# Kernel optimization log

Hardware: AMD Instinct MI355X
Metric: run time of the kernel (lower is better)

## Reference

```python
import jax, jax.numpy as jnp
import numpy as np

N_NODES = 40000
N_EDGES = 640000
IN_C = 128
HID = 32
HEADS = 4
OUT_C = 8
NUM_GRAPHS = 64
NEG_SLOPE = 0.2


def setup_inputs() -> dict:
    key = jax.random.key(0)
    ks = jax.random.split(key, 16)
    x = jax.random.normal(ks[0], (N_NODES, IN_C), dtype=jnp.float32)
    edge_index = jax.random.randint(ks[1], (2, N_EDGES), 0, N_NODES, dtype=jnp.int64)
    batch = jnp.sort(jax.random.randint(ks[2], (N_NODES,), 0, NUM_GRAPHS, dtype=jnp.int64))
    s = lambda k, shape, fan_in: jax.random.normal(k, shape, jnp.float32) / np.sqrt(fan_in)
    # conv0: in -> hid, 4 heads, concat
    W0 = s(ks[3], (IN_C, HEADS * HID), IN_C)
    a_src0 = s(ks[4], (HEADS, HID), HID)
    a_dst0 = s(ks[5], (HEADS, HID), HID)
    b0 = jnp.zeros((HEADS * HID,), jnp.float32)
    # conv1: hid*H -> hid, 4 heads, concat
    W1 = s(ks[6], (HEADS * HID, HEADS * HID), HEADS * HID)
    a_src1 = s(ks[7], (HEADS, HID), HID)
    a_dst1 = s(ks[8], (HEADS, HID), HID)
    b1 = jnp.zeros((HEADS * HID,), jnp.float32)
    # conv2: hid*H -> hid, 1 head, no concat
    W2 = s(ks[9], (HEADS * HID, HID), HEADS * HID)
    a_src2 = s(ks[10], (1, HID), HID)
    a_dst2 = s(ks[11], (1, HID), HID)
    b2 = jnp.zeros((HID,), jnp.float32)
    lin1_w = s(ks[12], (HID, IN_C), HID)
    lin1_b = jnp.zeros((IN_C,), jnp.float32)
    lin2_w = s(ks[13], (IN_C, OUT_C), IN_C)
    lin2_b = jnp.zeros((OUT_C,), jnp.float32)
    return dict(x=x, edge_index=edge_index, batch=batch,
                W0=W0, a_src0=a_src0, a_dst0=a_dst0, b0=b0,
                W1=W1, a_src1=a_src1, a_dst1=a_dst1, b1=b1,
                W2=W2, a_src2=a_src2, a_dst2=a_dst2, b2=b2,
                lin1_w=lin1_w, lin1_b=lin1_b, lin2_w=lin2_w, lin2_b=lin2_b)


def gat_conv(x, src, dst, W, a_src, a_dst, b, heads, out_c, concat):
    N = x.shape[0]
    h = (x @ W).reshape(N, heads, out_c)          # [N,H,C]
    als = (h * a_src[None]).sum(-1)               # [N,H]
    ald = (h * a_dst[None]).sum(-1)               # [N,H]
    e = jax.nn.leaky_relu(als[src] + ald[dst], NEG_SLOPE)  # [E,H]
    m = jax.ops.segment_max(e, dst, num_segments=N)
    m = jnp.where(jnp.isfinite(m), m, 0.0)
    p = jnp.exp(e - m[dst])                       # [E,H]
    denom = jax.ops.segment_sum(p, dst, num_segments=N)
    alpha = p / jnp.maximum(denom[dst], 1e-16)
    out = jax.ops.segment_sum(h[src] * alpha[:, :, None], dst, num_segments=N)
    out = out.reshape(N, heads * out_c) if concat else out.mean(axis=1)
    return out + b


def reference(x, edge_index, batch,
              W0, a_src0, a_dst0, b0,
              W1, a_src1, a_dst1, b1,
              W2, a_src2, a_dst2, b2,
              lin1_w, lin1_b, lin2_w, lin2_b):
    N = x.shape[0]
    # PyG GATConv adds self-loops by default
    loop = jnp.arange(N, dtype=edge_index.dtype)
    src = jnp.concatenate([edge_index[0], loop])
    dst = jnp.concatenate([edge_index[1], loop])
    # eval mode: dropout is identity
    h = jax.nn.elu(gat_conv(x, src, dst, W0, a_src0, a_dst0, b0, HEADS, HID, True))
    h = jax.nn.elu(gat_conv(h, src, dst, W1, a_src1, a_dst1, b1, HEADS, HID, True))
    h = jax.nn.elu(gat_conv(h, src, dst, W2, a_src2, a_dst2, b2, 1, HID, False))
    # global mean pool over graphs
    sums = jax.ops.segment_sum(h, batch, num_segments=NUM_GRAPHS)
    cnts = jax.ops.segment_sum(jnp.ones((N, 1), h.dtype), batch, num_segments=NUM_GRAPHS)
    g = sums / jnp.maximum(cnts, 1.0)             # [G, HID]
    g = jax.nn.relu(g @ lin1_w + lin1_b)
    return g @ lin2_w + lin2_b                    # [G, OUT_C]
```

## Files before the change

kernel.cpp:

```cpp
#include <hip/hip_runtime.h>
#include <hip/hip_bf16.h>

#define N_NODES 40000
#define N_EDGES 640000
#define E_TOT   (N_EDGES + N_NODES)
#define NUM_GRAPHS 64
#define CAP_SHIFT 6

#define CVTX_BLOCKS 5000
#define CVTW_BLOCKS 144
#define CVT_BLOCKS (CVTX_BLOCKS + CVTW_BLOCKS)
#define EBLOCKS ((E_TOT + 255) / 256)
#define GEMM_BLOCKS 625

typedef __attribute__((ext_vector_type(8))) short bf16x8;
typedef __attribute__((ext_vector_type(4))) float f32x4;

__device__ inline float bf2f(unsigned short u) {
    union { unsigned int i; float f; } v; v.i = ((unsigned int)u) << 16; return v.f;
}
__device__ inline unsigned short f2bf(float f) {
    union { float f; unsigned int i; } v; v.f = f;
    unsigned int r = v.i + 0x7FFF + ((v.i >> 16) & 1);
    return (unsigned short)(r >> 16);
}


__global__ __launch_bounds__(256) void cvt_kernel(const float* __restrict__ x,
                                                  const float* __restrict__ W0,
                                                  const float* __restrict__ W1,
                                                  const float* __restrict__ W2,
                                                  unsigned short* __restrict__ Xb,
                                                  unsigned short* __restrict__ Wt0,
                                                  unsigned short* __restrict__ Wt1,
                                                  unsigned short* __restrict__ Wt2) {
    int b = blockIdx.x;
    int tid = threadIdx.x;
    if (b < CVTX_BLOCKS) {
        int i = b * 256 + tid;
        float4 v = ((const float4*)x)[i];
        ushort4 o;
        o.x = f2bf(v.x); o.y = f2bf(v.y); o.z = f2bf(v.z); o.w = f2bf(v.w);
        ((ushort4*)Xb)[i] = o;
    } else {
        int idx = (b - CVTX_BLOCKS) * 256 + tid;
        if (idx < 16384) {
            int n = idx >> 7, k = idx & 127;
            Wt0[idx] = f2bf(W0[k * 128 + n]);
        } else if (idx < 32768) {
            int i = idx - 16384;
            int n = i >> 7, k = i & 127;
            Wt1[i] = f2bf(W1[k * 128 + n]);
        } else if (idx < 36864) {
            int i = idx - 32768;
            int n = i >> 7, k = i & 127;
            Wt2[i] = f2bf(W2[k * 32 + n]);
        }
    }
}


__device__ __forceinline__ void gemm128_body(int blk,
                                             const unsigned short* __restrict__ Xb,
                                             const unsigned short* __restrict__ Wt,
                                             const float* __restrict__ asrc,
                                             const float* __restrict__ adst,
                                             unsigned short* __restrict__ Hb,
                                             float* __restrict__ ALS_t,
                                             float* __restrict__ ALD_t) {
    int wave = threadIdx.x >> 6;
    int lane = threadIdx.x & 63;
    int l15 = lane & 15;
    int q = lane >> 4;
    int r0 = (blk * 4 + wave) * 16;

    f32x4 acc[8];
#pragma unroll
    for (int t = 0; t < 8; ++t) acc[t] = (f32x4){0.f, 0.f, 0.f, 0.f};

    float asv[8], adv[8];
#pragma unroll
    for (int t = 0; t < 8; ++t) {
        int c = t * 16 + l15;
        asv[t] = asrc[c];
        adv[t] = adst[c];
    }

    const unsigned short* xrow = Xb + (long)(r0 + l15) * 128 + q * 8;
    const unsigned short* wrow = Wt + (long)l15 * 128 + q * 8;
#pragma unroll
    for (int kt = 0; kt < 4; ++kt) {
        bf16x8 a = *(const bf16x8*)(xrow + kt * 32);
#pragma unroll
        for (int t = 0; t < 8; ++t) {
            bf16x8 b = *(const bf16x8*)(wrow + (long)t * 16 * 128 + kt * 32);
            acc[t] = __builtin_amdgcn_mfma_f32_16x16x32_bf16(a, b, acc[t], 0, 0, 0);
        }
    }

#pragma unroll
    for (int t = 0; t < 8; ++t)
#pragma unroll
        for (int i = 0; i < 4; ++i)
            Hb[(long)(r0 + q * 4 + i) * 128 + t * 16 + l15] = f2bf(acc[t][i]);

#pragma unroll
    for (int i = 0; i < 4; ++i) {
        float ps0 = acc[0][i] * asv[0] + acc[1][i] * asv[1];
        float ps1 = acc[2][i] * asv[2] + acc[3][i] * asv[3];
        float ps2 = acc[4][i] * asv[4] + acc[5][i] * asv[5];
        float ps3 = acc[6][i] * asv[6] + acc[7][i] * asv[7];
        float pd0 = acc[0][i] * adv[0] + acc[1][i] * adv[1];
        float pd1 = acc[2][i] * adv[2] + acc[3][i] * adv[3];
        float pd2 = acc[4][i] * adv[4] + acc[5][i] * adv[5];
        float pd3 = acc[6][i] * adv[6] + acc[7][i] * adv[7];
#pragma unroll
        for (int m = 1; m < 16; m <<= 1) {
            ps0 += __shfl_xor(ps0, m, 16); ps1 += __shfl_xor(ps1, m, 16);
            ps2 += __shfl_xor(ps2, m, 16); ps3 += __shfl_xor(ps3, m, 16);
            pd0 += __shfl_xor(pd0, m, 16); pd1 += __shfl_xor(pd1, m, 16);
            pd2 += __shfl_xor(pd2, m, 16); pd3 += __shfl_xor(pd3, m, 16);
        }
        int r = r0 + q * 4 + i;
        if (l15 < 4) {
            float v = (l15 == 0) ? ps0 : (l15 == 1) ? ps1 : (l15 == 2) ? ps2 : ps3;
            ALS_t[l15 * N_NODES + r] = v;
        } else if (l15 < 8) {
            int h = l15 - 4;
            float v = (h == 0) ? pd0 : (h == 1) ? pd1 : (h == 2) ? pd2 : pd3;
            ALD_t[h * N_NODES + r] = v;
        }
    }
}


__global__ __launch_bounds__(256) void gemm_scatter_kernel(const unsigned short* __restrict__ Xb,
                                                           const unsigned short* __restrict__ Wt,
                                                           const float* __restrict__ asrc,
                                                           const float* __restrict__ adst,
                                                           unsigned short* __restrict__ Hb,
                                                           float* __restrict__ ALS_t,
                                                           float* __restrict__ ALD_t,
                                                           const int* __restrict__ esrc,
                                                           const int* __restrict__ edst,
                                                           int* __restrict__ cnt,
                                                           int* __restrict__ psrc) {
    int b = blockIdx.x;
    if (b < GEMM_BLOCKS) {
        gemm128_body(b, Xb, Wt, asrc, adst, Hb, ALS_t, ALD_t);
    } else {
        int e = (b - GEMM_BLOCKS) * 256 + threadIdx.x;
        if (e < E_TOT) {
            int d, s;
            if (e < N_EDGES) { d = edst[e]; s = esrc[e]; }
            else             { d = e - N_EDGES; s = d; }
            int slot = atomicAdd(&cnt[d], 1);
            psrc[(d << CAP_SHIFT) + slot] = s;
        }
    }
}

__global__ __launch_bounds__(256) void gemm128_mfma(const unsigned short* __restrict__ Xb,
                                                    const unsigned short* __restrict__ Wt,
                                                    const float* __restrict__ asrc,
                                                    const float* __restrict__ adst,
                                                    unsigned short* __restrict__ Hb,
                                                    float* __restrict__ ALS_t,
                                                    float* __restrict__ ALD_t) {
    gemm128_body(blockIdx.x, Xb, Wt, asrc, adst, Hb, ALS_t, ALD_t);
}

__global__ __launch_bounds__(256) void gemm32_mfma(const unsigned short* __restrict__ Xb,
                                                   const unsigned short* __restrict__ Wt2,
                                                   const float* __restrict__ asrc,
                                                   const float* __restrict__ adst,
                                                   unsigned short* __restrict__ H2b,
                                                   float* __restrict__ ALS,
                                                   float* __restrict__ ALD) {
    int wave = threadIdx.x >> 6;
    int lane = threadIdx.x & 63;
    int l15 = lane & 15;
    int q = lane >> 4;
    int r0 = (blockIdx.x * 4 + wave) * 16;

    f32x4 acc[2];
    acc[0] = (f32x4){0.f, 0.f, 0.f, 0.f};
    acc[1] = (f32x4){0.f, 0.f, 0.f, 0.f};

    const unsigned short* xrow = Xb + (long)(r0 + l15) * 128 + q * 8;
    const unsigned short* wrow = Wt2 + (long)l15 * 128 + q * 8;
#pragma unroll
    for (int kt = 0; kt < 4; ++kt) {
        bf16x8 a = *(const bf16x8*)(xrow + kt * 32);
#pragma unroll
        for (int t = 0; t < 2; ++t) {
            bf16x8 b = *(const bf16x8*)(wrow + (long)t * 16 * 128 + kt * 32);
            acc[t] = __builtin_amdgcn_mfma_f32_16x16x32_bf16(a, b, acc[t], 0, 0, 0);
        }
    }

    float as0 = asrc[l15], as1 = asrc[16 + l15];
    float ad0 = adst[l15], ad1 = adst[16 + l15];
#pragma unroll
    for (int t = 0; t < 2; ++t)
#pragma unroll
        for (int i = 0; i < 4; ++i)
            H2b[(long)(r0 + q * 4 + i) * 32 + t * 16 + l15] = f2bf(acc[t][i]);

#pragma unroll
    for (int i = 0; i < 4; ++i) {
        float ps = acc[0][i] * as0 + acc[1][i] * as1;
        float pd = acc[0][i] * ad0 + acc[1][i] * ad1;
#pragma unroll
        for (int m = 1; m < 16; m <<= 1) {
            ps += __shfl_xor(ps, m, 16);
            pd += __shfl_xor(pd, m, 16);
        }
        if (l15 == 0) {
            int r = r0 + q * 4 + i;
            ALS[r] = ps;
            ALD[r] = pd;
        }
    }
}

__global__ __launch_bounds__(256) void agg128(const unsigned short* __restrict__ Hb,
                                              const float* __restrict__ ALS_t,
                                              const float* __restrict__ ALD_t,
                                              const int* __restrict__ cnt,
                                              const int* __restrict__ psrc,
                                              const float* __restrict__ bias,
                                              unsigned short* __restrict__ OUTb) {
    int n = blockIdx.x * 4 + (threadIdx.x >> 6);
    n = __builtin_amdgcn_readfirstlane(n);
    if (n >= N_NODES) return;
    int lane = threadIdx.x & 63;
    int c = lane * 2;
    int head = lane >> 4;
    int e16 = lane & 15;
    float aldh = ALD_t[head * N_NODES + n];
    const float* alsh = ALS_t + (long)head * N_NODES;
    int j0 = n << CAP_SHIFT;
    int j1 = j0 + __builtin_amdgcn_readfirstlane(cnt[n]);
    float a0 = 0.f, a1 = 0.f, dsum = 0.f;
    for (int jb = j0; jb < j1; jb += 16) {
        int j = jb + e16;
        int jc = (j < j1) ? j : (j1 - 1);
        int s = psrc[jc];
        float e = alsh[s] + aldh;
        e = (e > 0.f) ? e : 0.2f * e;
        float w = (j < j1) ? __expf(e) : 0.f;
        int st[16]; float wt[16];
#pragma unroll
        for (int t = 0; t < 16; ++t) {
            st[t] = __shfl(s, t, 16);
            wt[t] = __shfl(w, t, 16);
        }
        unsigned int hv[16];
#pragma unroll
        for (int t = 0; t < 16; ++t)
            hv[t] = *(const unsigned int*)(Hb + (long)st[t] * 128 + c);
#pragma unroll
        for (int t = 0; t < 16; ++t) {
            float h0 = bf2f((unsigned short)(hv[t] & 0xFFFF));
            float h1 = bf2f((unsigned short)(hv[t] >> 16));
            dsum += wt[t];
            a0 += wt[t] * h0;
            a1 += wt[t] * h1;
        }
    }
    float inv = 1.0f / dsum;
    float o0 = a0 * inv + bias[c];
    float o1 = a1 * inv + bias[c + 1];
    o0 = (o0 > 0.f) ? o0 : (__expf(o0) - 1.f);
    o1 = (o1 > 0.f) ? o1 : (__expf(o1) - 1.f);
    ushort2 ob; ob.x = f2bf(o0); ob.y = f2bf(o1);
    *(ushort2*)(OUTb + (long)n * 128 + c) = ob;
}

__global__ __launch_bounds__(256) void agg32(const unsigned short* __restrict__ H2b,
                                             const float* __restrict__ ALS,
                                             const float* __restrict__ ALD,
                                             const int* __restrict__ cnt,
                                             const int* __restrict__ psrc,
                                             const float* __restrict__ bias,
                                             float* __restrict__ OUT) {
    int wv = blockIdx.x * 4 + (threadIdx.x >> 6);
    int lane = threadIdx.x & 63;
    int col = lane & 31;
    int half = lane >> 5;
    int e16 = lane & 15;
    int n = wv * 2 + half;
    if (n >= N_NODES) return;
    float aldn = ALD[n];
    int j0 = n << CAP_SHIFT;
    int j1 = j0 + cnt[n];
    float a = 0.f, dsum = 0.f;
    for (int jb = j0; jb < j1; jb += 16) {
        int j = jb + e16;
        int jc = (j < j1) ? j : (j1 - 1);
        int s = psrc[jc];
        float e = ALS[s] + aldn;
        e = (e > 0.f) ? e : 0.2f * e;
        float w = (j < j1) ? __expf(e) : 0.f;
        int st[16]; float wt[16];
#pragma unroll
        for (int t = 0; t < 16; ++t) {
            st[t] = __shfl(s, t, 16);
            wt[t] = __shfl(w, t, 16);
        }
        unsigned short hv[16];
#pragma unroll
        for (int t = 0; t < 16; ++t)
            hv[t] = H2b[st[t] * 32 + col];
#pragma unroll
        for (int t = 0; t < 16; ++t) {
            dsum += wt[t];
            a += wt[t] * bf2f(hv[t]);
        }
    }
    float o = a / dsum + bias[col];
    o = (o > 0.f) ? o : (__expf(o) - 1.f);
    OUT[n * 32 + col] = o;
}

__global__ __launch_bounds__(256) void pool_kernel(const float* __restrict__ H3,
                                                   const int* __restrict__ batch,
                                                   float* __restrict__ gsum,
                                                   float* __restrict__ gcnt) {
    const int CHUNK = 40;
    int gid = (blockIdx.x * 256 + threadIdx.x) >> 5;
    int c = threadIdx.x & 31;
    int n0 = gid * CHUNK;
    if (n0 >= N_NODES) return;
    int n1 = n0 + CHUNK;
    if (n1 > N_NODES) n1 = N_NODES;
    int cur = batch[n0];
    float acc = 0.f;
    int cnt = 0;
    for (int n = n0; n < n1; ++n) {
        int b = batch[n];
        if (b != cur) {
            atomicAdd(&gsum[cur * 32 + c], acc);
            if (c == 0) atomicAdd(&gcnt[cur], (float)cnt);
            cur = b; acc = 0.f; cnt = 0;
        }
        acc += H3[n * 32 + c];
        cnt++;
    }
    atomicAdd(&gsum[cur * 32 + c], acc);
    if (c == 0) atomicAdd(&gcnt[cur], (float)cnt);
}

__global__ __launch_bounds__(256) void mlp_kernel(const float* __restrict__ gsum,
                                                  const float* __restrict__ gcnt,
                                                  const float* __restrict__ l1w,
                                                  const float* __restrict__ l1b,
                                                  const float* __restrict__ l2w,
                                                  const float* __restrict__ l2b,
                                                  float* __restrict__ out) {
    __shared__ float g[NUM_GRAPHS * 32];
    __shared__ float t1[NUM_GRAPHS * 128];
    int tid = threadIdx.x;
    for (int i = tid; i < NUM_GRAPHS * 32; i += 256) {
        float c = gcnt[i >> 5];
        g[i] = gsum[i] / fmaxf(c, 1.0f);
    }
    __syncthreads();
    for (int i = tid; i < NUM_GRAPHS * 128; i += 256) {
        int r = i >> 7, j = i & 127;
        float a = l1b[j];
        for (int k = 0; k < 32; ++k) a += g[r * 32 + k] * l1w[k * 128 + j];
        t1[i] = fmaxf(a, 0.f);
    }
    __syncthreads();
    for (int i = tid; i < NUM_GRAPHS * 8; i += 256) {
        int r = i >> 3, j = i & 7;
        float a = l2b[j];
        for (int k = 0; k < 128; ++k) a += t1[r * 128 + k] * l2w[k * 8 + j];
        out[i] = a;
    }
}


extern "C" void kernel_launch(void* const* d_in, const int* in_sizes, int n_in,
                              void* d_out, int out_size, void* d_ws, size_t ws_size,
                              hipStream_t stream) {
    const float* x      = (const float*)d_in[0];
    const int*   eidx   = (const int*)d_in[1];
    const int*   batch  = (const int*)d_in[2];
    const float* W0     = (const float*)d_in[3];
    const float* asrc0  = (const float*)d_in[4];
    const float* adst0  = (const float*)d_in[5];
    const float* b0     = (const float*)d_in[6];
    const float* W1     = (const float*)d_in[7];
    const float* asrc1  = (const float*)d_in[8];
    const float* adst1  = (const float*)d_in[9];
    const float* b1     = (const float*)d_in[10];
    const float* W2     = (const float*)d_in[11];
    const float* asrc2  = (const float*)d_in[12];
    const float* adst2  = (const float*)d_in[13];
    const float* b2     = (const float*)d_in[14];
    const float* l1w    = (const float*)d_in[15];
    const float* l1b    = (const float*)d_in[16];
    const float* l2w    = (const float*)d_in[17];
    const float* l2b    = (const float*)d_in[18];
    float* out = (float*)d_out;

    const int* esrc = eidx;
    const int* edst = eidx + N_EDGES;

    float* ALS  = (float*)d_ws;
    float* ALD  = ALS + N_NODES * 4;
    float* h3   = ALD + N_NODES * 4;
    int* cnt    = (int*)(h3 + (long)N_NODES * 32);
    float* gsum = (float*)(cnt + N_NODES);
    float* gcnt = gsum + NUM_GRAPHS * 32;
    int* psrc   = (int*)(gcnt + NUM_GRAPHS);
    uintptr_t p = (uintptr_t)(psrc + ((long)N_NODES << CAP_SHIFT));
    p = (p + 15) & ~(uintptr_t)15;
    unsigned short* Xb   = (unsigned short*)p;
    unsigned short* Hb   = Xb + (long)N_NODES * 128;
    unsigned short* OUTb = Hb + (long)N_NODES * 128;
    unsigned short* H2b  = OUTb + (long)N_NODES * 128;
    unsigned short* Wt0  = H2b + (long)N_NODES * 32;
    unsigned short* Wt1  = Wt0 + 128 * 128;
    unsigned short* Wt2  = Wt1 + 128 * 128;

    size_t zbytes = (size_t)(N_NODES + NUM_GRAPHS * 32 + NUM_GRAPHS) * 4;
    hipMemsetAsync(cnt, 0, zbytes, stream);

    cvt_kernel<<<CVT_BLOCKS, 256, 0, stream>>>(x, W0, W1, W2, Xb, Wt0, Wt1, Wt2);

    gemm_scatter_kernel<<<GEMM_BLOCKS + EBLOCKS, 256, 0, stream>>>(
        Xb, Wt0, asrc0, adst0, Hb, ALS, ALD, esrc, edst, cnt, psrc);
    agg128<<<10000, 256, 0, stream>>>(Hb, ALS, ALD, cnt, psrc, b0, OUTb);

    gemm128_mfma<<<GEMM_BLOCKS, 256, 0, stream>>>(OUTb, Wt1, asrc1, adst1, Hb, ALS, ALD);
    agg128<<<10000, 256, 0, stream>>>(Hb, ALS, ALD, cnt, psrc, b1, OUTb);

    gemm32_mfma<<<GEMM_BLOCKS, 256, 0, stream>>>(OUTb, Wt2, asrc2, adst2, H2b, ALS, ALD);
    agg32<<<5000, 256, 0, stream>>>(H2b, ALS, ALD, cnt, psrc, b2, h3);

    pool_kernel<<<125, 256, 0, stream>>>(h3, batch, gsum, gcnt);
    mlp_kernel<<<1, 256, 0, stream>>>(gsum, gcnt, l1w, l1b, l2w, l2b, out);
}
```

Before: 290.1 us.

## Narrow source-index list to 16-bit and widen agg128 gathers to 8 bytes

The per-destination source list is stored as unsigned short instead of int. This halves its write and read traffic, and is valid because node ids stay below 65536. agg128 is restructured so each lane gathers four bf16 features with a uint2 load, and the two 32-lane halves of the wave handle alternate edges; partial sums are combined with a cross-half shuffle. This cuts the number of gather instructions and the fp32 unpacking per edge, in exchange for an extra reduction and idle lanes in the epilogue.

```diff
diff --git a/kernel.cpp b/kernel.cpp
--- a/kernel.cpp
+++ b/kernel.cpp
@@ -144,7 +144,7 @@
                                                            const int* __restrict__ esrc,
                                                            const int* __restrict__ edst,
                                                            int* __restrict__ cnt,
-                                                           int* __restrict__ psrc) {
+                                                           unsigned short* __restrict__ psrc) {
     int b = blockIdx.x;
     if (b < GEMM_BLOCKS) {
         gemm128_body(b, Xb, Wt, asrc, adst, Hb, ALS_t, ALD_t);
@@ -155,7 +155,7 @@
             if (e < N_EDGES) { d = edst[e]; s = esrc[e]; }
             else             { d = e - N_EDGES; s = d; }
             int slot = atomicAdd(&cnt[d], 1);
-            psrc[(d << CAP_SHIFT) + slot] = s;
+            psrc[(d << CAP_SHIFT) + slot] = (unsigned short)s;
         }
     }
 }
@@ -228,21 +228,24 @@
                                               const float* __restrict__ ALS_t,
                                               const float* __restrict__ ALD_t,
                                               const int* __restrict__ cnt,
-                                              const int* __restrict__ psrc,
+                                              const unsigned short* __restrict__ psrc,
                                               const float* __restrict__ bias,
                                               unsigned short* __restrict__ OUTb) {
     int n = blockIdx.x * 4 + (threadIdx.x >> 6);
     n = __builtin_amdgcn_readfirstlane(n);
     if (n >= N_NODES) return;
     int lane = threadIdx.x & 63;
-    int c = lane * 2;
-    int head = lane >> 4;
     int e16 = lane & 15;
-    float aldh = ALD_t[head * N_NODES + n];
-    const float* alsh = ALS_t + (long)head * N_NODES;
+    int hh = lane >> 4;
+    int half = lane >> 5;
+    int c4 = (lane & 31) * 4;
+    int hgrp = (lane & 31) >> 3;
+    float aldh = ALD_t[hh * N_NODES + n];
+    const float* alsh = ALS_t + (long)hh * N_NODES;
     int j0 = n << CAP_SHIFT;
     int j1 = j0 + __builtin_amdgcn_readfirstlane(cnt[n]);
-    float a0 = 0.f, a1 = 0.f, dsum = 0.f;
+    float a0 = 0.f, a1 = 0.f, a2 = 0.f, a3 = 0.f, dsum = 0.f;
+    int wsrc = hgrp * 16 + half;
     for (int jb = j0; jb < j1; jb += 16) {
         int j = jb + e16;
         int jc = (j < j1) ? j : (j1 - 1);
@@ -250,39 +253,45 @@
         float e = alsh[s] + aldh;
         e = (e > 0.f) ? e : 0.2f * e;
         float w = (j < j1) ? __expf(e) : 0.f;
-        int st[16]; float wt[16];
-#pragma unroll
-        for (int t = 0; t < 16; ++t) {
-            st[t] = __shfl(s, t, 16);
-            wt[t] = __shfl(w, t, 16);
-        }
-        unsigned int hv[16];
-#pragma unroll
-        for (int t = 0; t < 16; ++t)
-            hv[t] = *(const unsigned int*)(Hb + (long)st[t] * 128 + c);
-#pragma unroll
-        for (int t = 0; t < 16; ++t) {
-            float h0 = bf2f((unsigned short)(hv[t] & 0xFFFF));
-            float h1 = bf2f((unsigned short)(hv[t] >> 16));
-            dsum += wt[t];
-            a0 += wt[t] * h0;
-            a1 += wt[t] * h1;
-        }
-    }
-    float inv = 1.0f / dsum;
-    float o0 = a0 * inv + bias[c];
-    float o1 = a1 * inv + bias[c + 1];
-    o0 = (o0 > 0.f) ? o0 : (__expf(o0) - 1.f);
-    o1 = (o1 > 0.f) ? o1 : (__expf(o1) - 1.f);
-    ushort2 ob; ob.x = f2bf(o0); ob.y = f2bf(o1);
-    *(ushort2*)(OUTb + (long)n * 128 + c) = ob;
+        dsum += w;
+#pragma unroll
+        for (int t = 0; t < 8; ++t) {
+            int se = __shfl(s, t * 2 + half, 16);
+            uint2 hv = *(const uint2*)(Hb + (long)se * 128 + c4);
+            float wv = __shfl(w, wsrc + t * 2);
+            a0 += wv * bf2f((unsigned short)(hv.x & 0xFFFF));
+            a1 += wv * bf2f((unsigned short)(hv.x >> 16));
+            a2 += wv * bf2f((unsigned short)(hv.y & 0xFFFF));
+            a3 += wv * bf2f((unsigned short)(hv.y >> 16));
+        }
+    }
+    a0 += __shfl_xor(a0, 32); a1 += __shfl_xor(a1, 32);
+    a2 += __shfl_xor(a2, 32); a3 += __shfl_xor(a3, 32);
+#pragma unroll
+    for (int m = 1; m < 16; m <<= 1) dsum += __shfl_xor(dsum, m, 16);
+    float dsv = __shfl(dsum, hgrp * 16);
+    if (half == 0) {
+        float inv = 1.0f / dsv;
+        float4 bv = *(const float4*)(bias + c4);
+        float o0 = a0 * inv + bv.x;
+        float o1 = a1 * inv + bv.y;
+        float o2 = a2 * inv + bv.z;
+        float o3 = a3 * inv + bv.w;
+        o0 = (o0 > 0.f) ? o0 : (__expf(o0) - 1.f);
+        o1 = (o1 > 0.f) ? o1 : (__expf(o1) - 1.f);
+        o2 = (o2 > 0.f) ? o2 : (__expf(o2) - 1.f);
+        o3 = (o3 > 0.f) ? o3 : (__expf(o3) - 1.f);
+        ushort4 ov;
+        ov.x = f2bf(o0); ov.y = f2bf(o1); ov.z = f2bf(o2); ov.w = f2bf(o3);
+        *(ushort4*)(OUTb + (long)n * 128 + c4) = ov;
+    }
 }
 
 __global__ __launch_bounds__(256) void agg32(const unsigned short* __restrict__ H2b,
                                              const float* __restrict__ ALS,
                                              const float* __restrict__ ALD,
                                              const int* __restrict__ cnt,
-                                             const int* __restrict__ psrc,
+                                             const unsigned short* __restrict__ psrc,
                                              const float* __restrict__ bias,
                                              float* __restrict__ OUT) {
     int wv = blockIdx.x * 4 + (threadIdx.x >> 6);
@@ -416,7 +425,7 @@
     int* cnt    = (int*)(h3 + (long)N_NODES * 32);
     float* gsum = (float*)(cnt + N_NODES);
     float* gcnt = gsum + NUM_GRAPHS * 32;
-    int* psrc   = (int*)(gcnt + NUM_GRAPHS);
+    unsigned short* psrc = (unsigned short*)(gcnt + NUM_GRAPHS);
     uintptr_t p = (uintptr_t)(psrc + ((long)N_NODES << CAP_SHIFT));
     p = (p + 15) & ~(uintptr_t)15;
     unsigned short* Xb   = (unsigned short*)p;
```

Result: slower. 299.2 us (+3.1%).
